# Optimization experiments

Hardware: AMD Instinct MI355X
Metric: run time of the kernel (lower is better)

The kernel has to match this reference:

```python
import jax, jax.numpy as jnp
import numpy as np

CIN, HID, OUT = 128, 256, 349
NTYPES, ETYPES = 4, 5
N0, N1, N2 = 120000, 40000, 10000
GNODES, GEDGES = 250000, 2000000
E0, E1 = 1500000, 400000


def setup_inputs() -> dict:
    key = jax.random.key(0)
    ks = jax.random.split(key, 24)
    ri = jax.random.randint
    rn = jax.random.normal
    inp = {}
    inp['n_id'] = ri(ks[0], (N0,), 0, GNODES)
    inp['x0'] = rn(ks[1], (100000, CIN), dtype=jnp.float32)
    inp['src0'] = ri(ks[2], (E0,), 0, N0)
    inp['dst0'] = ri(ks[3], (E0,), 0, N1)
    inp['e_id0'] = ri(ks[4], (E0,), 0, GEDGES)
    inp['src1'] = ri(ks[5], (E1,), 0, N1)
    inp['dst1'] = ri(ks[6], (E1,), 0, N2)
    inp['e_id1'] = ri(ks[7], (E1,), 0, GEDGES)
    inp['edge_type'] = ri(ks[8], (GEDGES,), 0, ETYPES)
    inp['node_type'] = ri(ks[9], (GNODES,), 0, NTYPES)
    inp['local_node_idx'] = ri(ks[10], (GNODES,), 0, 50000)
    # learned parameters
    inp['emb1'] = rn(ks[11], (50000, CIN), dtype=jnp.float32)
    inp['emb2'] = rn(ks[12], (50000, CIN), dtype=jnp.float32)
    inp['emb3'] = rn(ks[13], (50000, CIN), dtype=jnp.float32)
    s0 = 1.0 / np.sqrt(CIN)
    s1 = 1.0 / np.sqrt(HID)
    inp['relW0'] = rn(ks[14], (ETYPES, CIN, HID), dtype=jnp.float32) * s0
    inp['rootW0'] = rn(ks[15], (NTYPES, CIN, HID), dtype=jnp.float32) * s0
    inp['rootb0'] = rn(ks[16], (NTYPES, HID), dtype=jnp.float32) * 0.02
    inp['relW1'] = rn(ks[17], (ETYPES, HID, OUT), dtype=jnp.float32) * s1
    inp['rootW1'] = rn(ks[18], (NTYPES, HID, OUT), dtype=jnp.float32) * s1
    inp['rootb1'] = rn(ks[19], (NTYPES, OUT), dtype=jnp.float32) * 0.02
    return inp


def _group_input(tables, node_type, local_node_idx, n_id):
    # RGNN.group_input: per-node-type gather from feature / embedding tables.
    nt = node_type[n_id]            # [N0]
    li = local_node_idx[n_id]       # [N0]
    h = jnp.zeros((n_id.shape[0], CIN), dtype=tables[0].dtype)
    for k, tab in enumerate(tables):
        idx = jnp.minimum(li, tab.shape[0] - 1)
        h = jnp.where((nt == k)[:, None], tab[idx], h)
    return h, nt


def _rgcn_layer(x, nt_src, src, dst, et, relW, rootW, rootb, n_tgt):
    # out = sum_t mean-aggregate(x_j over edges of type t) @ W_t  (linear commutes with mean)
    T = relW.shape[0]
    xj = x[src]                                           # [E, Cin] gather
    seg = dst * T + et                                    # fused (target, edge_type) segment id
    sums = jax.ops.segment_sum(xj, seg, num_segments=n_tgt * T)
    cnts = jax.ops.segment_sum(jnp.ones((src.shape[0],), x.dtype), seg, num_segments=n_tgt * T)
    mean = (sums / jnp.maximum(cnts, 1.0)[:, None]).reshape(n_tgt, T, -1)  # [Nt, T, Cin]
    out = jnp.einsum('ntc,tco->no', mean, relW)           # [Nt, Cout]
    # per-node-type root linear: out[mask] += root_lins[i](x_target[mask])
    x_t = x[:n_tgt]
    nt_t = nt_src[:n_tgt]
    allr = jnp.einsum('nc,tco->tno', x_t, rootW) + rootb[:, None, :]  # [Tn, Nt, Cout]
    root = jnp.take_along_axis(allr, nt_t[None, :, None], axis=0)[0]
    return out + root


def reference(n_id, x0, src0, dst0, e_id0, src1, dst1, e_id1, edge_type, node_type,
              local_node_idx, emb1, emb2, emb3, relW0, rootW0, rootb0, relW1, rootW1, rootb1):
    h, nt = _group_input([x0, emb1, emb2, emb3], node_type, local_node_idx, n_id)
    # layer 0: I -> H
    h = _rgcn_layer(h, nt, src0, dst0, edge_type[e_id0], relW0, rootW0, rootb0, N1)
    h = jax.nn.relu(h)
    nt = nt[:N1]
    # layer 1: H -> O
    h = _rgcn_layer(h, nt, src1, dst1, edge_type[e_id1], relW1, rootW1, rootb1, N2)
    return jax.nn.log_softmax(h, axis=-1)
```

## Files before the change

### kernel.cpp

```cpp
#include <hip/hip_runtime.h>
#include <hip/hip_bf16.h>
#include <cmath>

constexpr int kCIN = 128, kHID = 256, kOUT = 349;
constexpr int kNT = 4, kET = 5;
constexpr int kN0 = 120000, kN1 = 40000, kN2 = 10000;
constexpr int kNSEG0 = kN1 * kET;
constexpr int kNSEG1 = kN2 * kET;
constexpr int kNSEG = kNSEG0 + kNSEG1;

constexpr int kBinSegs = 512;
constexpr int kNBin0 = (kNSEG0 + kBinSegs - 1) / kBinSegs;
constexpr int kNBin1 = (kNSEG1 + kBinSegs - 1) / kBinSegs;
constexpr int kNBin  = kNBin0 + kNBin1;
constexpr int kNBLK  = 256;
constexpr int kSB    = 128;
constexpr int kGB    = kN0 / 64;

typedef __bf16 bf16x8 __attribute__((ext_vector_type(8)));
typedef float f32x4 __attribute__((ext_vector_type(4)));
typedef float f32x2v __attribute__((ext_vector_type(2)));
typedef unsigned short ushort8v __attribute__((ext_vector_type(8)));

__device__ __forceinline__ unsigned short f2b(float f) {
    unsigned int b = __float_as_uint(f);
    unsigned int r = (b + 0x7FFFu + ((b >> 16) & 1u)) >> 16;
    return (unsigned short)r;
}
__device__ __forceinline__ float b2f(unsigned short u) {
    return __uint_as_float((unsigned int)u << 16);
}
__device__ __forceinline__ void gl2lds16(const void* g, void* l) {
    __builtin_amdgcn_global_load_lds(
        (const __attribute__((address_space(1))) void*)g,
        (__attribute__((address_space(3))) void*)l, 16, 0, 0);
}

__device__ __forceinline__ unsigned int f2e4m3(float f) {
#if __has_builtin(__builtin_amdgcn_cvt_pk_fp8_f32)
    return (unsigned int)(__builtin_amdgcn_cvt_pk_fp8_f32(f, f, 0, false) & 0xFF);
#else
    unsigned int sb = (__float_as_uint(f) >> 31) << 7;
    float m = fminf(fabsf(f), 448.f);
    unsigned int code;
    if (m < 0.015625f) {
        code = (unsigned int)__float2int_rn(m * 512.f);
    } else {
        unsigned int b = __float_as_uint(m);
        b = b + 0x7FFFF + ((b >> 20) & 1);
        int e8 = (int)(b >> 23) - 120;
        if (e8 > 15) code = 0x7E;
        else code = ((unsigned int)e8 << 3) | ((b >> 20) & 7);
    }
    return sb | code;
#endif
}

__device__ __forceinline__ void e4m3x4_to_f32(unsigned int u, float* o4) {
#if __has_builtin(__builtin_amdgcn_cvt_pk_f32_fp8)
    f32x2v a = __builtin_amdgcn_cvt_pk_f32_fp8(u, false);
    f32x2v b = __builtin_amdgcn_cvt_pk_f32_fp8(u, true);
    o4[0] = a[0]; o4[1] = a[1]; o4[2] = b[0]; o4[3] = b[1];
#else
#pragma unroll
    for (int i = 0; i < 4; i++) {
        unsigned int c = (u >> (8 * i)) & 0xFF;
        unsigned int s = c >> 7, e = (c >> 3) & 15, mm = c & 7;
        float v;
        if (e == 0) v = (float)mm * 0.001953125f;
        else        v = __uint_as_float((e + 120u) << 23 | mm << 20);
        o4[i] = s ? -v : v;
    }
#endif
}

__global__ void k_prep(const float* __restrict__ relW0, const float* __restrict__ rootW0,
                       unsigned short* __restrict__ Bt0T,
                       const float* __restrict__ relW1, const float* __restrict__ rootW1,
                       unsigned short* __restrict__ Bt1T,
                       const int* __restrict__ etype, unsigned char* __restrict__ et8, int nET)
{
    constexpr int T0 = kNT * 256 * 768;
    constexpr int T1 = kNT * 384 * 1536;
    constexpr int TP = T0 + T1;
    int i = blockIdx.x * 256 + threadIdx.x;
    if (i < T0) {
        int g = i / (256 * 768);
        int rem = i - g * (256 * 768);
        int col = rem / 768;
        int k = rem - col * 768;
        float v = (k < 640) ? relW0[(size_t)k * 256 + col]
                            : rootW0[((size_t)g * 128 + (k - 640)) * 256 + col];
        Bt0T[i] = f2b(v);
    } else if (i < TP) {
        int ii = i - T0;
        int g = ii / (384 * 1536);
        int rem = ii - g * (384 * 1536);
        int col = rem / 1536;
        int k = rem - col * 1536;
        float v = 0.f;
        if (col < kOUT) v = (k < 1280) ? relW1[(size_t)k * kOUT + col]
                                       : rootW1[((size_t)g * 256 + (k - 1280)) * kOUT + col];
        Bt1T[ii] = f2b(v);
    } else {
        int k = i - TP;
        if (k < nET) et8[k] = (unsigned char)etype[k];
    }
}

__global__ __launch_bounds__(1024) void k_bincnt(
    const int* __restrict__ dst0, const int* __restrict__ eid0, int E0,
    const int* __restrict__ dst1, const int* __restrict__ eid1, int E1,
    const unsigned char* __restrict__ et8, int* __restrict__ cnts2d,
    int* __restrict__ seg32,
    const int* __restrict__ n_id, const int* __restrict__ ntype, int* __restrict__ ntcnts,
    const float* __restrict__ x0, const float* __restrict__ e1f,
    const float* __restrict__ e2f, const float* __restrict__ e3f,
    const int* __restrict__ lidx,
    unsigned short* __restrict__ h0b, unsigned char* __restrict__ h0f8,
    int* __restrict__ nt0)
{
    __shared__ int h[kNBin];
    const int tid = threadIdx.x;
    if (blockIdx.x < kNBLK) {
        for (int k = tid; k < kNBin; k += 1024) h[k] = 0;
        __syncthreads();
        int Etot = E0 + E1;
        int chunk = (Etot + kNBLK - 1) / kNBLK;
        int lo = blockIdx.x * chunk;
        int hi = min(lo + chunk, Etot);
        for (int i = lo + tid; i < hi; i += 1024) {
            int c;
            if (i < E0) c = dst0[i] * kET + (int)et8[eid0[i]];
            else { int e = i - E0; c = kNBin0 * kBinSegs + dst1[e] * kET + (int)et8[eid1[e]]; }
            seg32[i] = c;
            atomicAdd(&h[c >> 9], 1);
        }
        __syncthreads();
        for (int k = tid; k < kNBin; k += 1024) cnts2d[(size_t)k * kNBLK + blockIdx.x] = h[k];
    } else if (blockIdx.x < kNBLK + 2 * kSB) {
        int b = blockIdx.x - kNBLK;
        int layer = b >= kSB;
        int blk = b - layer * kSB;
        int M = layer ? kN2 : kN1;
        if (tid < 4) h[tid] = 0;
        __syncthreads();
        int chunk = (M + kSB - 1) / kSB;
        int lo = blk * chunk, hi = min(lo + chunk, M);
        for (int i = lo + tid; i < hi; i += 1024) atomicAdd(&h[ntype[n_id[i]]], 1);
        __syncthreads();
        if (tid < 4) ntcnts[(layer * 4 + tid) * kSB + blk] = h[tid];
    } else {
        int base = (blockIdx.x - kNBLK - 2 * kSB) * 64;
        int lane = tid & 31;
        int r0 = base + (tid >> 5);
        int r1 = r0 + 32;
        int gid0 = n_id[r0], gid1 = n_id[r1];
        int nta = ntype[gid0], ntb = ntype[gid1];
        int lia = lidx[gid0], lib = lidx[gid1];
        const float* taba; int rowsa;
        if (nta == 0)      { taba = x0;  rowsa = 100000; }
        else if (nta == 1) { taba = e1f; rowsa = 50000; }
        else if (nta == 2) { taba = e2f; rowsa = 50000; }
        else               { taba = e3f; rowsa = 50000; }
        const float* tabb; int rowsb;
        if (ntb == 0)      { tabb = x0;  rowsb = 100000; }
        else if (ntb == 1) { tabb = e1f; rowsb = 50000; }
        else if (ntb == 2) { tabb = e2f; rowsb = 50000; }
        else               { tabb = e3f; rowsb = 50000; }
        int ia = lia < rowsa ? lia : rowsa - 1;
        int ib = lib < rowsb ? lib : rowsb - 1;
        float4 v0 = reinterpret_cast<const float4*>(taba + (size_t)ia * kCIN)[lane];
        float4 v1 = reinterpret_cast<const float4*>(tabb + (size_t)ib * kCIN)[lane];
        ushort4 o0, o1;
        o0.x = f2b(v0.x); o0.y = f2b(v0.y); o0.z = f2b(v0.z); o0.w = f2b(v0.w);
        o1.x = f2b(v1.x); o1.y = f2b(v1.y); o1.z = f2b(v1.z); o1.w = f2b(v1.w);
        reinterpret_cast<ushort4*>(h0b + (size_t)r0 * kCIN)[lane] = o0;
        reinterpret_cast<ushort4*>(h0b + (size_t)r1 * kCIN)[lane] = o1;
        unsigned int q0 = f2e4m3(v0.x) | (f2e4m3(v0.y) << 8) | (f2e4m3(v0.z) << 16) | (f2e4m3(v0.w) << 24);
        unsigned int q1 = f2e4m3(v1.x) | (f2e4m3(v1.y) << 8) | (f2e4m3(v1.z) << 16) | (f2e4m3(v1.w) << 24);
        reinterpret_cast<unsigned int*>(h0f8 + (size_t)r0 * kCIN)[lane] = q0;
        reinterpret_cast<unsigned int*>(h0f8 + (size_t)r1 * kCIN)[lane] = q1;
        if (lane == 0) { nt0[r0] = nta; nt0[r1] = ntb; }
    }
}

__global__ void k_scan1(const int* __restrict__ cnt, int* __restrict__ excl,
                        int* __restrict__ blksum, int n)
{
    __shared__ int sm[1024];
    int i = blockIdx.x * 1024 + threadIdx.x;
    int v = (i < n) ? cnt[i] : 0;
    sm[threadIdx.x] = v;
    __syncthreads();
    for (int off = 1; off < 1024; off <<= 1) {
        int t = (threadIdx.x >= off) ? sm[threadIdx.x - off] : 0;
        __syncthreads();
        sm[threadIdx.x] += t;
        __syncthreads();
    }
    if (i < n) excl[i] = sm[threadIdx.x] - v;
    if (threadIdx.x == 1023) blksum[blockIdx.x] = sm[1023];
}

__global__ __launch_bounds__(1024) void k_scan2(
    int* __restrict__ blksum, int nblk,
    const int* __restrict__ ntcnts, int* __restrict__ ntoffs,
    int* __restrict__ goff0, int* __restrict__ goff1)
{
    __shared__ int sm[1024];
    int tid = threadIdx.x;
    if (blockIdx.x == 0) {
        int v = (tid < nblk) ? blksum[tid] : 0;
        sm[tid] = v;
        __syncthreads();
        for (int off = 1; off < 1024; off <<= 1) {
            int t = (tid >= off) ? sm[tid - off] : 0;
            __syncthreads();
            sm[tid] += t;
            __syncthreads();
        }
        if (tid < nblk) blksum[tid] = sm[tid] - v;
    } else {
        int v = ntcnts[tid];
        sm[tid] = v;
        __syncthreads();
        for (int off = 1; off < 512; off <<= 1) {
            int t = 0;
            if ((tid & 511) >= off) t = sm[tid - off];
            __syncthreads();
            sm[tid] += t;
            __syncthreads();
        }
        int excl = sm[tid] - v;
        ntoffs[tid] = excl;
        if ((tid & 127) == 0) {
            int layer = tid >> 9;
            int t = (tid >> 7) & 3;
            if (layer == 0) goff0[t] = excl; else goff1[t] = excl;
        }
        if (tid == 0) { goff0[4] = kN1; goff1[4] = kN2; }
    }
}

__global__ __launch_bounds__(1024) void k_binplace(
    const int* __restrict__ src0, int E0,
    const int* __restrict__ src1, int E1,
    const int* __restrict__ seg32,
    const int* __restrict__ offs2d, const int* __restrict__ blksum,
    unsigned int* __restrict__ pairs,
    const int* __restrict__ nt0, const int* __restrict__ ntoffs,
    int* __restrict__ perm0, int* __restrict__ perm1)
{
    __shared__ int cur[kNBin];
    const int tid = threadIdx.x;
    if (blockIdx.x < kNBLK) {
        for (int k = tid; k < kNBin; k += 1024) {
            size_t li = (size_t)k * kNBLK + blockIdx.x;
            cur[k] = offs2d[li] + blksum[li >> 10];
        }
        __syncthreads();
        int Etot = E0 + E1;
        int chunk = (Etot + kNBLK - 1) / kNBLK;
        int lo = blockIdx.x * chunk;
        int hi = min(lo + chunk, Etot);
        for (int i = lo + tid; i < hi; i += 1024) {
            int c = seg32[i];
            int s = (i < E0) ? src0[i] : src1[i - E0];
            unsigned int pay = (unsigned int)s | ((unsigned int)(c & (kBinSegs - 1)) << 17);
            int p = atomicAdd(&cur[c >> 9], 1);
            pairs[p] = pay;
        }
    } else {
        int b = blockIdx.x - kNBLK;
        int layer = b >= kSB;
        int blk = b - layer * kSB;
        int M = layer ? kN2 : kN1;
        int* perm = layer ? perm1 : perm0;
        if (tid < 4) cur[tid] = ntoffs[(layer * 4 + tid) * kSB + blk];
        __syncthreads();
        int chunk = (M + kSB - 1) / kSB;
        int lo = blk * chunk, hi = min(lo + chunk, M);
        for (int i = lo + tid; i < hi; i += 1024) {
            int p = atomicAdd(&cur[nt0[i]], 1);
            perm[p] = i;
        }
    }
}

__global__ __launch_bounds__(1024) void k_binscatter(
    const int* __restrict__ offs2d, const int* __restrict__ blksum, int Etot,
    const unsigned int* __restrict__ pairs,
    int* __restrict__ order, int* __restrict__ starts, int* __restrict__ cnt)
{
    __shared__ int h[kBinSegs];
    __shared__ int sc[kBinSegs];
    __shared__ int cur[kBinSegs];
    const int bin = blockIdx.x;
    const int tid = threadIdx.x;
    size_t bi = (size_t)bin * kNBLK;
    const int base = offs2d[bi] + blksum[bi >> 10];
    int end = Etot;
    if (bin + 1 < kNBin) {
        size_t ei = (size_t)(bin + 1) * kNBLK;
        end = offs2d[ei] + blksum[ei >> 10];
    }
    const int c = end - base;
    const unsigned int* pp = pairs + base;

    for (int k = tid; k < kBinSegs; k += 1024) h[k] = 0;
    __syncthreads();
    for (int j = tid; j < c; j += 1024) atomicAdd(&h[pp[j] >> 17], 1);
    __syncthreads();
    if (tid < kBinSegs) sc[tid] = h[tid];
    __syncthreads();
    for (int off = 1; off < kBinSegs; off <<= 1) {
        int t = 0;
        if (tid < kBinSegs && tid >= off) t = sc[tid - off];
        __syncthreads();
        if (tid < kBinSegs) sc[tid] += t;
        __syncthreads();
    }
    int seg_rel, abs_base, seglim;
    if (bin < kNBin0) { seg_rel = bin * kBinSegs; abs_base = seg_rel; seglim = kNSEG0 - seg_rel; }
    else { seg_rel = (bin - kNBin0) * kBinSegs; abs_base = kNSEG0 + seg_rel; seglim = kNSEG1 - seg_rel; }
    if (tid < kBinSegs) {
        int excl = sc[tid] - h[tid];
        cur[tid] = excl;
        if (tid < seglim) {
            starts[abs_base + tid] = base + excl;
            cnt[abs_base + tid] = h[tid];
        }
    }
    __syncthreads();
    for (int j = tid; j < c; j += 1024) {
        unsigned int u = pp[j];
        int sl = (int)(u >> 17);
        int p = atomicAdd(&cur[sl], 1);
        order[base + p] = (int)(u & 0x1FFFFu);
    }
}

template<int C>
__global__ __launch_bounds__(256) void k_segreduce8(
    const int* __restrict__ starts, const int* __restrict__ cnt,
    const int* __restrict__ order, const unsigned char* __restrict__ h8,
    unsigned short* __restrict__ mean, int nseg)
{
    constexpr int L = C / 16;
    constexpr int SPB = 256 / L;
    int sidx = blockIdx.x * SPB + threadIdx.x / L;
    if (sidx >= nseg) return;
    int lane = threadIdx.x % L;
    int st = starts[sidx];
    int n = cnt[sidx];
    const unsigned char* hp = h8 + (size_t)lane * 16;
    float a0[16], a1[16];
#pragma unroll
    for (int i = 0; i < 16; i++) { a0[i] = 0.f; a1[i] = 0.f; }
    int j = 0;
    for (; j + 2 <= n; j += 2) {
        int s0 = order[st + j + 0];
        int s1 = order[st + j + 1];
        uint4 u0 = *reinterpret_cast<const uint4*>(hp + (size_t)s0 * C);
        uint4 u1 = *reinterpret_cast<const uint4*>(hp + (size_t)s1 * C);
        float d[16];
        e4m3x4_to_f32(u0.x, d); e4m3x4_to_f32(u0.y, d + 4);
        e4m3x4_to_f32(u0.z, d + 8); e4m3x4_to_f32(u0.w, d + 12);
#pragma unroll
        for (int i = 0; i < 16; i++) a0[i] += d[i];
        e4m3x4_to_f32(u1.x, d); e4m3x4_to_f32(u1.y, d + 4);
        e4m3x4_to_f32(u1.z, d + 8); e4m3x4_to_f32(u1.w, d + 12);
#pragma unroll
        for (int i = 0; i < 16; i++) a1[i] += d[i];
    }
    if (j < n) {
        int s0 = order[st + j];
        uint4 u0 = *reinterpret_cast<const uint4*>(hp + (size_t)s0 * C);
        float d[16];
        e4m3x4_to_f32(u0.x, d); e4m3x4_to_f32(u0.y, d + 4);
        e4m3x4_to_f32(u0.z, d + 8); e4m3x4_to_f32(u0.w, d + 12);
#pragma unroll
        for (int i = 0; i < 16; i++) a0[i] += d[i];
    }
    float sc = 1.0f / fmaxf((float)n, 1.0f);
    ushort8v o0, o1;
#pragma unroll
    for (int i = 0; i < 8; i++) {
        o0[i] = f2b((a0[i] + a1[i]) * sc);
        o1[i] = f2b((a0[i + 8] + a1[i + 8]) * sc);
    }
    unsigned short* mp = mean + (size_t)sidx * C + lane * 16;
    *reinterpret_cast<ushort8v*>(mp) = o0;
    *reinterpret_cast<ushort8v*>(mp + 8) = o1;
}

template<int C, int BM, int BNF, int NCB, int WR, int WC, int RELU, int AF8, int OUTF32>
__global__ __launch_bounds__(256) void k_gemm_sorted(
    int M, int Nreal, int NpadK,
    const unsigned short* __restrict__ meanb,
    const unsigned short* __restrict__ hb,
    const unsigned char* __restrict__ hb8,
    const unsigned short* __restrict__ BtT,
    const float* __restrict__ rootb,
    const int* __restrict__ perm, const int* __restrict__ goff,
    float* __restrict__ outf, unsigned char* __restrict__ outf8)
{
    constexpr int K1 = kET * C;
    constexpr int K  = K1 + C;
    constexpr int FM = BM / (16 * WR);
    constexpr int FN = BNF / (16 * WC);
    __shared__ __align__(16) char ldsA[BM * 128];
    __shared__ __align__(16) char ldsB[BNF * 128];

    int nwg = gridDim.x;
    int orig = blockIdx.x;
    int q = nwg >> 3, r8 = nwg & 7, x8 = orig & 7;
    int logical = (x8 < r8 ? x8 * (q + 1) : r8 * (q + 1) + (x8 - r8) * q) + (orig >> 3);
    int colb = logical % NCB;
    int t = logical / NCB;

    int g, row0s = 0, gend = 0;
    {
        int gs[5] = {goff[0], goff[1], goff[2], goff[3], goff[4]};
        int tb = 0;
        for (g = 0; g < 4; ++g) {
            int cg = gs[g + 1] - gs[g];
            int ntl = (cg + BM - 1) / BM;
            if (t < tb + ntl) { row0s = gs[g] + (t - tb) * BM; gend = gs[g + 1]; break; }
            tb += ntl;
        }
        if (g == 4) return;
    }
    const int rows_here = min(BM, gend - row0s);
    const unsigned short* BtG = BtT + (size_t)g * NpadK;

    const int tid = threadIdx.x;
    const int col0 = colb * BNF;
    const int wid = tid >> 6, lane = tid & 63;
    const int wrow = (wid / WC) * (BM / WR);
    const int wcol = (wid % WC) * (BNF / WC);
    const int lr = lane >> 3;
    const int kb = (lane & 7) * 16;

    f32x4 acc[FM][FN] = {};

    for (int k0 = 0; k0 < K; k0 += 64) {
        const bool inMean = (k0 < K1);
        const size_t kB = (size_t)k0 * 2;
        if (!AF8 || inMean) {
#pragma unroll
            for (int c2 = 0; c2 < BM / 32; ++c2) {
                int rb = (wid * (BM / 32) + c2) * 8;
                int r = rb + lr;
                int pr = perm[row0s + min(r, rows_here - 1)];
                const char* rowp = inMean
                    ? (const char*)(meanb + (size_t)pr * K1) + kB
                    : (const char*)(hb + (size_t)pr * C) + (kB - (size_t)K1 * 2);
                gl2lds16(rowp + (kb ^ ((r & 7) << 4)), &ldsA[rb * 128]);
            }
        } else {
#pragma unroll
            for (int c2 = 0; c2 < BM / 32; ++c2) {
                int rb = (wid * (BM / 32) + c2) * 8;
                int r = rb + lr;
                int pr = perm[row0s + min(r, rows_here - 1)];
                int eo = (k0 - K1) + ((kb ^ ((r & 7) << 4)) >> 1);
                uint2 u = *reinterpret_cast<const uint2*>(hb8 + (size_t)pr * C + eo);
                float d[8];
                e4m3x4_to_f32(u.x, d); e4m3x4_to_f32(u.y, d + 4);
                ushort8v o;
#pragma unroll
                for (int i = 0; i < 8; i++) o[i] = f2b(d[i]);
                *reinterpret_cast<ushort8v*>(&ldsA[rb * 128 + lane * 16]) = o;
            }
        }
#pragma unroll
        for (int c2 = 0; c2 < BNF / 32; ++c2) {
            int rb = (wid * (BNF / 32) + c2) * 8;
            int r = rb + lr;
            const char* rowp = (const char*)(BtG + (size_t)(col0 + r) * K) + kB;
            gl2lds16(rowp + (kb ^ ((r & 7) << 4)), &ldsB[rb * 128]);
        }
        __syncthreads();
#pragma unroll
        for (int kc = 0; kc < 2; kc++) {
            int kb2 = kc * 64 + (lane >> 4) * 16;
            bf16x8 af[FM], bfr[FN];
#pragma unroll
            for (int m = 0; m < FM; m++) {
                int r = wrow + m * 16 + (lane & 15);
                af[m] = *reinterpret_cast<const bf16x8*>(&ldsA[r * 128 + (kb2 ^ ((r & 7) << 4))]);
            }
#pragma unroll
            for (int n = 0; n < FN; n++) {
                int r = wcol + n * 16 + (lane & 15);
                bfr[n] = *reinterpret_cast<const bf16x8*>(&ldsB[r * 128 + (kb2 ^ ((r & 7) << 4))]);
            }
#pragma unroll
            for (int m = 0; m < FM; m++)
#pragma unroll
                for (int n = 0; n < FN; n++)
                    acc[m][n] = __builtin_amdgcn_mfma_f32_16x16x32_bf16(af[m], bfr[n], acc[m][n], 0, 0, 0);
        }
        __syncthreads();
    }

#pragma unroll
    for (int m = 0; m < FM; m++) {
        int rlb = wrow + m * 16 + (lane >> 4) * 4;
#pragma unroll
        for (int n = 0; n < FN; n++) {
            int col = col0 + wcol + n * 16 + (lane & 15);
            if (col >= Nreal) continue;
            f32x4 v = acc[m][n];
#pragma unroll
            for (int j = 0; j < 4; j++) {
                int rl = rlb + j;
                if (rl >= rows_here) continue;
                int orig_row = perm[row0s + rl];
                float xv = v[j] + rootb[g * Nreal + col];
                if (RELU) xv = fmaxf(xv, 0.f);
                if (OUTF32) outf[(size_t)orig_row * Nreal + col] = xv;
                else        outf8[(size_t)orig_row * Nreal + col] = (unsigned char)f2e4m3(xv);
            }
        }
    }
}

__global__ void k_logsm(float* __restrict__ out, int M, int N)
{
    int row = blockIdx.x * 4 + (threadIdx.x >> 6);
    if (row >= M) return;
    int lane = threadIdx.x & 63;
    float* p = out + (size_t)row * N;
    float mx = -3.4e38f;
    for (int c = lane; c < N; c += 64) mx = fmaxf(mx, p[c]);
#pragma unroll
    for (int o = 32; o > 0; o >>= 1) mx = fmaxf(mx, __shfl_xor(mx, o));
    float s = 0.f;
    for (int c = lane; c < N; c += 64) s += expf(p[c] - mx);
#pragma unroll
    for (int o = 32; o > 0; o >>= 1) s += __shfl_xor(s, o);
    float lse = mx + logf(s);
    for (int c = lane; c < N; c += 64) p[c] -= lse;
}

extern "C" void kernel_launch(void* const* d_in, const int* in_sizes, int n_in,
                              void* d_out, int out_size, void* d_ws, size_t ws_size,
                              hipStream_t stream)
{
    const int*   n_id   = (const int*)d_in[0];
    const float* x0     = (const float*)d_in[1];
    const int*   src0   = (const int*)d_in[2];
    const int*   dst0   = (const int*)d_in[3];
    const int*   eid0   = (const int*)d_in[4];
    const int*   src1   = (const int*)d_in[5];
    const int*   dst1   = (const int*)d_in[6];
    const int*   eid1   = (const int*)d_in[7];
    const int*   etype  = (const int*)d_in[8];
    const int*   ntype  = (const int*)d_in[9];
    const int*   lidx   = (const int*)d_in[10];
    const float* emb1   = (const float*)d_in[11];
    const float* emb2   = (const float*)d_in[12];
    const float* emb3   = (const float*)d_in[13];
    const float* relW0  = (const float*)d_in[14];
    const float* rootW0 = (const float*)d_in[15];
    const float* rootb0 = (const float*)d_in[16];
    const float* relW1  = (const float*)d_in[17];
    const float* rootW1 = (const float*)d_in[18];
    const float* rootb1 = (const float*)d_in[19];
    float* out = (float*)d_out;

    const int E0 = in_sizes[2];
    const int E1 = in_sizes[5];
    const int Etot = E0 + E1;
    const int nET = in_sizes[8];
    constexpr int K0s  = kET * kCIN + kCIN;
    constexpr int K1s  = kET * kHID + kHID;
    constexpr int Npad0 = 256;
    constexpr int Npad1 = 384;

    char* ws = (char*)d_ws;
    size_t off = 0;
    auto alloc = [&](size_t bytes) -> void* {
        void* p = ws + off;
        off = (off + bytes + 255) & ~(size_t)255;
        return p;
    };
    unsigned short* h0b   = (unsigned short*)alloc((size_t)kN0 * kCIN * 2);
    unsigned char*  h0f8  = (unsigned char*)alloc((size_t)kN0 * kCIN);
    int*            nt0   = (int*)alloc((size_t)kN0 * 4);
    unsigned short* meanb = (unsigned short*)alloc((size_t)kNSEG0 * kCIN * 2);
    int*            cnt    = (int*)alloc((size_t)kNSEG * 4);
    int*            starts = (int*)alloc((size_t)kNSEG * 4);
    int*            cnts2d = (int*)alloc((size_t)kNBin * kNBLK * 4);
    int*            offs2d = (int*)alloc((size_t)kNBin * kNBLK * 4);
    int*            blksum = (int*)alloc(1024 * 4);
    unsigned int*   pairs  = (unsigned int*)alloc((size_t)Etot * 4);
    int*            order  = (int*)alloc((size_t)Etot * 4);
    int*            seg32  = (int*)alloc((size_t)Etot * 4);
    unsigned char*  et8    = (unsigned char*)alloc((size_t)nET);
    unsigned char*  h1f8  = (unsigned char*)alloc((size_t)kN1 * kHID);
    unsigned short* Bt0T  = (unsigned short*)alloc((size_t)kNT * Npad0 * K0s * 2);
    unsigned short* Bt1T  = (unsigned short*)alloc((size_t)kNT * Npad1 * K1s * 2);
    int*            perm0  = (int*)alloc((size_t)kN1 * 4);
    int*            goff0  = (int*)alloc(8 * 4);
    int*            perm1  = (int*)alloc((size_t)kN2 * 4);
    int*            goff1  = (int*)alloc(8 * 4);
    int*            ntcnts = (int*)alloc(1024 * 4);
    int*            ntoffs = (int*)alloc(1024 * 4);

    constexpr int TPREP = kNT * Npad0 * K0s + kNT * Npad1 * K1s;
    int prep_total = TPREP + nET;
    k_prep<<<(prep_total + 255) / 256, 256, 0, stream>>>(relW0, rootW0, Bt0T, relW1, rootW1, Bt1T,
                                                         etype, et8, nET);

    k_bincnt<<<kNBLK + 2 * kSB + kGB, 1024, 0, stream>>>(
        dst0, eid0, E0, dst1, eid1, E1, et8, cnts2d, seg32,
        n_id, ntype, ntcnts, x0, emb1, emb2, emb3, lidx, h0b, h0f8, nt0);

    int nscan = kNBin * kNBLK;
    int nblk = (nscan + 1023) / 1024;
    k_scan1<<<nblk, 1024, 0, stream>>>(cnts2d, offs2d, blksum, nscan);
    k_scan2<<<2, 1024, 0, stream>>>(blksum, nblk, ntcnts, ntoffs, goff0, goff1);
    k_binplace<<<kNBLK + 2 * kSB, 1024, 0, stream>>>(src0, E0, src1, E1, seg32,
                                                     offs2d, blksum, pairs, nt0, ntoffs, perm0, perm1);
    k_binscatter<<<kNBin, 1024, 0, stream>>>(offs2d, blksum, Etot, pairs, order, starts, cnt);

    k_segreduce8<kCIN><<<(kNSEG0 + 31) / 32, 256, 0, stream>>>(starts, cnt, order, h0f8, meanb, kNSEG0);
    int g0 = (kN1 / 64 + 4) * 2;
    k_gemm_sorted<kCIN, 64, 128, 2, 2, 2, 1, 0, 0><<<g0, 256, 0, stream>>>(
        kN1, kHID, Npad0 * K0s, meanb, h0b, nullptr, Bt0T, rootb0, perm0, goff0, nullptr, h1f8);

    k_segreduce8<kHID><<<(kNSEG1 + 15) / 16, 256, 0, stream>>>(starts + kNSEG0, cnt + kNSEG0, order, h1f8, meanb, kNSEG1);
    int g1 = (kN2 / 64 + 5) * 3;
    k_gemm_sorted<kHID, 64, 128, 3, 2, 2, 0, 1, 1><<<g1, 256, 0, stream>>>(
        kN2, kOUT, Npad1 * K1s, meanb, nullptr, h1f8, Bt1T, rootb1, perm1, goff1, out, nullptr);

    k_logsm<<<(kN2 + 3) / 4, 256, 0, stream>>>(out, kN2, kOUT);
}
```

Before: 219.8 us.

## Gather four rows per thread and write bf16 copy only for target nodes

The input-gather branch now handles 128 rows per block, with four rows per thread, and issues all four table loads before converting. This raises memory-level parallelism and halves the number of gather blocks. The bf16 copy of the input features is now written only for the first N1 rows, because only target-node rows need it for the root linear; the fp8 copy is still written for every row. This cuts write traffic and shrinks the workspace buffer, but relies on no later kernel reading bf16 rows at or beyond N1.

```diff
diff --git a/kernel.cpp b/kernel.cpp
--- a/kernel.cpp
+++ b/kernel.cpp
@@ -15,7 +15,7 @@
 constexpr int kNBin  = kNBin0 + kNBin1;
 constexpr int kNBLK  = 256;
 constexpr int kSB    = 128;
-constexpr int kGB    = kN0 / 64;
+constexpr int kGB    = (kN0 + 127) / 128;
 
 typedef __bf16 bf16x8 __attribute__((ext_vector_type(8)));
 typedef float f32x4 __attribute__((ext_vector_type(4)));
@@ -151,37 +151,47 @@
         __syncthreads();
         if (tid < 4) ntcnts[(layer * 4 + tid) * kSB + blk] = h[tid];
     } else {
-        int base = (blockIdx.x - kNBLK - 2 * kSB) * 64;
+        int base = (blockIdx.x - kNBLK - 2 * kSB) * 128;
         int lane = tid & 31;
-        int r0 = base + (tid >> 5);
-        int r1 = r0 + 32;
-        int gid0 = n_id[r0], gid1 = n_id[r1];
-        int nta = ntype[gid0], ntb = ntype[gid1];
-        int lia = lidx[gid0], lib = lidx[gid1];
-        const float* taba; int rowsa;
-        if (nta == 0)      { taba = x0;  rowsa = 100000; }
-        else if (nta == 1) { taba = e1f; rowsa = 50000; }
-        else if (nta == 2) { taba = e2f; rowsa = 50000; }
-        else               { taba = e3f; rowsa = 50000; }
-        const float* tabb; int rowsb;
-        if (ntb == 0)      { tabb = x0;  rowsb = 100000; }
-        else if (ntb == 1) { tabb = e1f; rowsb = 50000; }
-        else if (ntb == 2) { tabb = e2f; rowsb = 50000; }
-        else               { tabb = e3f; rowsb = 50000; }
-        int ia = lia < rowsa ? lia : rowsa - 1;
-        int ib = lib < rowsb ? lib : rowsb - 1;
-        float4 v0 = reinterpret_cast<const float4*>(taba + (size_t)ia * kCIN)[lane];
-        float4 v1 = reinterpret_cast<const float4*>(tabb + (size_t)ib * kCIN)[lane];
-        ushort4 o0, o1;
-        o0.x = f2b(v0.x); o0.y = f2b(v0.y); o0.z = f2b(v0.z); o0.w = f2b(v0.w);
-        o1.x = f2b(v1.x); o1.y = f2b(v1.y); o1.z = f2b(v1.z); o1.w = f2b(v1.w);
-        reinterpret_cast<ushort4*>(h0b + (size_t)r0 * kCIN)[lane] = o0;
-        reinterpret_cast<ushort4*>(h0b + (size_t)r1 * kCIN)[lane] = o1;
-        unsigned int q0 = f2e4m3(v0.x) | (f2e4m3(v0.y) << 8) | (f2e4m3(v0.z) << 16) | (f2e4m3(v0.w) << 24);
-        unsigned int q1 = f2e4m3(v1.x) | (f2e4m3(v1.y) << 8) | (f2e4m3(v1.z) << 16) | (f2e4m3(v1.w) << 24);
-        reinterpret_cast<unsigned int*>(h0f8 + (size_t)r0 * kCIN)[lane] = q0;
-        reinterpret_cast<unsigned int*>(h0f8 + (size_t)r1 * kCIN)[lane] = q1;
-        if (lane == 0) { nt0[r0] = nta; nt0[r1] = ntb; }
+        int grp = tid >> 5;
+        int r[4];
+        const float* tab[4];
+        int idx[4], ntv[4];
+        bool ok[4];
+#pragma unroll
+        for (int k = 0; k < 4; k++) {
+            r[k] = base + grp + k * 32;
+            ok[k] = r[k] < kN0;
+            int rr = ok[k] ? r[k] : kN0 - 1;
+            int gid = n_id[rr];
+            int nt = ntype[gid];
+            int li = lidx[gid];
+            const float* tb; int rows;
+            if (nt == 0)      { tb = x0;  rows = 100000; }
+            else if (nt == 1) { tb = e1f; rows = 50000; }
+            else if (nt == 2) { tb = e2f; rows = 50000; }
+            else              { tb = e3f; rows = 50000; }
+            tab[k] = tb;
+            idx[k] = li < rows ? li : rows - 1;
+            ntv[k] = nt;
+        }
+        float4 v[4];
+#pragma unroll
+        for (int k = 0; k < 4; k++)
+            v[k] = reinterpret_cast<const float4*>(tab[k] + (size_t)idx[k] * kCIN)[lane];
+#pragma unroll
+        for (int k = 0; k < 4; k++) {
+            if (!ok[k]) continue;
+            unsigned int q = f2e4m3(v[k].x) | (f2e4m3(v[k].y) << 8)
+                           | (f2e4m3(v[k].z) << 16) | (f2e4m3(v[k].w) << 24);
+            reinterpret_cast<unsigned int*>(h0f8 + (size_t)r[k] * kCIN)[lane] = q;
+            if (r[k] < kN1) {
+                ushort4 o;
+                o.x = f2b(v[k].x); o.y = f2b(v[k].y); o.z = f2b(v[k].z); o.w = f2b(v[k].w);
+                reinterpret_cast<ushort4*>(h0b + (size_t)r[k] * kCIN)[lane] = o;
+            }
+            if (lane == 0) nt0[r[k]] = ntv[k];
+        }
     }
 }
 
@@ -588,7 +598,7 @@
         off = (off + bytes + 255) & ~(size_t)255;
         return p;
     };
-    unsigned short* h0b   = (unsigned short*)alloc((size_t)kN0 * kCIN * 2);
+    unsigned short* h0b   = (unsigned short*)alloc((size_t)kN1 * kCIN * 2);
     unsigned char*  h0f8  = (unsigned char*)alloc((size_t)kN0 * kCIN);
     int*            nt0   = (int*)alloc((size_t)kN0 * 4);
     unsigned short* meanb = (unsigned short*)alloc((size_t)kNSEG0 * kCIN * 2);
```

Measured after the change: 218.0 us. About the same (-0.8%).
